# Optimization experiments

Measured on AMD Instinct MI355X. Metric: run time of the kernel, lower is better.

The kernel has to match this reference:

```python
import jax, jax.numpy as jnp
import numpy as np
from jax import lax

B, NBB, C, H, W = 32, 16, 1024, 22, 22
P = 3            # pooled output size (3x3)
SCALE = 1.0 / 16.0
EPS = 1e-5


def setup_inputs() -> dict:
    key = jax.random.key(0)
    ks = jax.random.split(key, 12)
    feat = jax.random.normal(ks[0], (B, C, H, W), jnp.float32)
    # bbox in xywh image coords, in-range for a 352x352 search region
    xy = jax.random.uniform(ks[1], (B, NBB, 2), jnp.float32, 0.0, 250.0)
    wh = jax.random.uniform(ks[2], (B, NBB, 2), jnp.float32, 16.0, 100.0)
    bbox = jnp.concatenate([xy, wh], axis=-1)
    conv_w = jax.random.normal(ks[3], (C, C, 3, 3), jnp.float32) * 0.01
    conv_b = jnp.zeros((C,), jnp.float32)
    bn_gamma = jnp.ones((C,), jnp.float32)
    bn_beta = jnp.zeros((C,), jnp.float32)
    bn_mean = jax.random.normal(ks[4], (C,), jnp.float32) * 0.1
    bn_var = jax.random.uniform(ks[5], (C,), jnp.float32, 0.5, 1.5)
    w1 = jax.random.normal(ks[6], (C // 2, C), jnp.float32) * 0.02
    b1 = jnp.zeros((C // 2,), jnp.float32)
    w2 = jax.random.normal(ks[7], (C // 2, C // 2), jnp.float32) * 0.02
    b2 = jnp.zeros((C // 2,), jnp.float32)
    w3 = jax.random.normal(ks[8], (512, C // 2), jnp.float32) * 0.02
    b3 = jnp.zeros((512,), jnp.float32)
    return dict(feat=feat, bbox=bbox, conv_w=conv_w, conv_b=conv_b,
                bn_gamma=bn_gamma, bn_beta=bn_beta, bn_mean=bn_mean, bn_var=bn_var,
                w1=w1, b1=b1, w2=w2, b2=b2, w3=w3, b3=b3)


def _hat_int(t):
    # Antiderivative of the bilinear hat h(u)=max(0,1-|u|), clipped to support.
    t = jnp.clip(t, -1.0, 1.0)
    return t + 0.5 - 0.5 * t * jnp.abs(t)


def _bin_weights(lo, bw, n):
    # lo, bw: [B, NBB].  Returns exact integral weights [B, NBB, P, n]:
    # W[b,r,p,i] = integral over bin p of hat(x - i) dx  (PrRoI closed form).
    p = jnp.arange(P, dtype=lo.dtype)
    xs = lo[..., None] + p * bw[..., None]          # [B,NBB,P] bin starts
    xe = xs + bw[..., None]                          # bin ends
    i = jnp.arange(n, dtype=lo.dtype)
    return _hat_int(xe[..., None] - i) - _hat_int(xs[..., None] - i)


def reference(feat, bbox, conv_w, conv_b, bn_gamma, bn_beta, bn_mean, bn_var,
              w1, b1, w2, b2, w3, b3):
    # --- PrRoI pooling (exact separable bilinear integral) ---
    x1 = bbox[..., 0] * SCALE
    y1 = bbox[..., 1] * SCALE
    x2 = (bbox[..., 0] + bbox[..., 2]) * SCALE
    y2 = (bbox[..., 1] + bbox[..., 3]) * SCALE
    bw = (x2 - x1) / P
    bh = (y2 - y1) / P
    Wx = _bin_weights(x1, bw, W)                     # [B,NBB,P,W]
    Wy = _bin_weights(y1, bh, H)                     # [B,NBB,P,H]
    pooled = jnp.einsum('bchw,bnqh,bnpw->bncqp', feat, Wy, Wx)  # [B,NBB,C,P,P]
    area = jnp.maximum(bw * bh, 0.0)[..., None, None, None]
    pooled = jnp.where(area > 0, pooled / jnp.maximum(area, 1e-12), 0.0)
    x = pooled.reshape(B * NBB, C, P, P)

    # --- conv_bn_relu: 3x3 conv, valid padding -> 1x1, BN (eval), ReLU ---
    x = lax.conv_general_dilated(x, conv_w, (1, 1), 'VALID',
                                 dimension_numbers=('NCHW', 'OIHW', 'NCHW'))
    x = x + conv_b[:, None, None]
    x = (x - bn_mean[:, None, None]) * (bn_gamma * lax.rsqrt(bn_var + EPS))[:, None, None]
    x = x + bn_beta[:, None, None]
    x = jax.nn.relu(x)

    # --- MLP head ---
    x = x.reshape(B * NBB, C)
    x = jax.nn.relu(x @ w1.T + b1)
    x = jax.nn.relu(x @ w2.T + b2)
    x = x @ w3.T + b3
    return x.reshape(B, NBB, 512)
```

## Files before the change

### kernel.cpp

```cpp
#include <hip/hip_runtime.h>
#include <hip/hip_bf16.h>

#define B_    32
#define NBB_  16
#define C_    1024
#define NROI  512
#define KCONV 9216
#define SCALE_ (1.0f/16.0f)
#define EPS_  1e-5f

using f32x4  = __attribute__((ext_vector_type(4))) float;
using bf16x8 = __attribute__((ext_vector_type(8))) short;

__device__ __forceinline__ unsigned f2bf(float f) {
  union { float f; unsigned u; } x; x.f = f;
  unsigned r = x.u + 0x7fffu + ((x.u >> 16) & 1u);
  return r >> 16;
}

__device__ __forceinline__ unsigned pk_bf16(float lo, float hi) {
  __hip_bfloat162 h = __float22bfloat162_rn(make_float2(lo, hi));
  return *reinterpret_cast<unsigned*>(&h);
}

__device__ __forceinline__ float hat_int(float t) {
  t = fminf(fmaxf(t, -1.f), 1.f);
  return t + 0.5f - 0.5f * t * fabsf(t);
}

__device__ __forceinline__ void glds16(const void* g, void* l) {
  __builtin_amdgcn_global_load_lds((const __attribute__((address_space(1))) void*)g,
                                   (__attribute__((address_space(3))) void*)l, 16, 0, 0);
}

__global__ __launch_bounds__(192) void prep_w2d(const float* __restrict__ bbox,
                                                unsigned short* __restrict__ W2d) {
  __shared__ float wyS[16*66], wxS[16*66];
  int b = blockIdx.x, tid = threadIdx.x;
  for (int t = tid; t < 352; t += 192) {
    int n = t / 22, i = t - n * 22;
    float4 bb = ((const float4*)bbox)[b*16 + n];
    float x1 = bb.x * SCALE_, y1 = bb.y * SCALE_;
    float x2 = (bb.x + bb.z) * SCALE_, y2 = (bb.y + bb.w) * SCALE_;
    float bw = (x2 - x1) / 3.f, bh = (y2 - y1) / 3.f;
    float area = fmaxf(bw * bh, 0.f);
    float inv = area > 0.f ? 1.f / fmaxf(area, 1e-12f) : 0.f;
    float fi = (float)i;
#pragma unroll
    for (int q = 0; q < 3; ++q) {
      float sy = y1 + q * bh;
      wyS[n*66 + q*22 + i] = hat_int(sy + bh - fi) - hat_int(sy - fi);
      float sx = x1 + q * bw;
      wxS[n*66 + q*22 + i] = (hat_int(sx + bw - fi) - hat_int(sx - fi)) * inv;
    }
  }
  __syncthreads();
  if (tid < 144) {
    int n = tid / 9, qp = tid - n*9, q = qp / 3, p = qp - q*3;
    const float* wyp = wyS + n*66 + q*22;
    const float* wxp = wxS + n*66 + p*22;
    unsigned short* out = W2d + ((size_t)b*144 + tid) * 512;
    for (int h = 0; h < 22; ++h) {
      float yv = wyp[h];
      int kb = h * 22;
#pragma unroll
      for (int w = 0; w < 22; w += 2)
        *(unsigned*)&out[kb + w] = pk_bf16(yv * wxp[w], yv * wxp[w+1]);
    }
#pragma unroll
    for (int k = 484; k < 512; k += 2) *(unsigned*)&out[k] = 0u;
  }
}

__global__ __launch_bounds__(256) void cvt3_bf16(const float* __restrict__ w1, const float* __restrict__ w2,
                                                 const float* __restrict__ w3,
                                                 unsigned short* __restrict__ o1, unsigned short* __restrict__ o2,
                                                 unsigned short* __restrict__ o3) {
  int i = blockIdx.x * 256 + threadIdx.x;
  const float* src; unsigned short* dst; int g;
  if (i < 65536)      { src = w1; dst = o1; g = i; }
  else if (i < 98304) { src = w2; dst = o2; g = i - 65536; }
  else                { src = w3; dst = o3; g = i - 98304; }
  float4 a = ((const float4*)src)[2*g];
  float4 b = ((const float4*)src)[2*g + 1];
  uint4 pk;
  pk.x = pk_bf16(a.x, a.y); pk.y = pk_bf16(a.z, a.w);
  pk.z = pk_bf16(b.x, b.y); pk.w = pk_bf16(b.z, b.w);
  ((uint4*)dst)[g] = pk;
}

__global__ __launch_bounds__(256) void convw_t(const float* __restrict__ cw,
                                               unsigned short* __restrict__ out) {
  __shared__ unsigned short T[9][1028];
  int o = blockIdx.x, tid = threadIdx.x;
  const float4* src = (const float4*)(cw + (size_t)o * 9216);
#pragma unroll
  for (int it = 0; it < 9; ++it) {
    int i = tid + it * 256;
    float4 v = src[i];
    int e = i * 4;
    { int c = e / 9,     qp = e - c*9;             T[qp][c] = (unsigned short)f2bf(v.x); }
    { int ee = e+1; int c = ee / 9, qp = ee - c*9; T[qp][c] = (unsigned short)f2bf(v.y); }
    { int ee = e+2; int c = ee / 9, qp = ee - c*9; T[qp][c] = (unsigned short)f2bf(v.z); }
    { int ee = e+3; int c = ee / 9, qp = ee - c*9; T[qp][c] = (unsigned short)f2bf(v.w); }
  }
  __syncthreads();
  unsigned short* dst = out + (size_t)o * 9216;
#pragma unroll
  for (int qp = 0; qp < 9; ++qp) {
    uint2 w = *(const uint2*)&T[qp][tid * 4];
    ((uint2*)(dst + qp * 1024))[tid] = w;
  }
}

__global__ __launch_bounds__(256) void cvt_feat(const float* __restrict__ feat,
                                                unsigned short* __restrict__ featB) {
  int blk = blockIdx.x;
  int tid = threadIdx.x;
  const float4* src = (const float4*)(feat + (size_t)blk * 16 * 484);
  unsigned short* dstB = featB + (size_t)blk * 16 * 512;
#pragma unroll
  for (int it = 0; it < 8; ++it) {
    int j = tid + it * 256;
    if (j < 1936) {
      float4 v = src[j];
      int lin = j * 4;
      int c = lin / 484, w = lin - c * 484;
      uint2 pk;
      pk.x = pk_bf16(v.x, v.y); pk.y = pk_bf16(v.z, v.w);
      *(uint2*)&dstB[(size_t)c * 512 + w] = pk;
    }
  }
  if (tid < 112) {
    int c = tid / 7, ws = tid - c * 7;
    uint2 z; z.x = 0u; z.y = 0u;
    *(uint2*)&dstB[(size_t)c * 512 + 484 + ws * 4] = z;
  }
}

__global__ __launch_bounds__(384) void pool_gemm(const unsigned short* __restrict__ W2d,
                                                 const unsigned short* __restrict__ featB,
                                                 unsigned short* __restrict__ X) {
  __shared__ __align__(16) unsigned short As[2][4608];
  __shared__ __align__(16) unsigned short Bs[2][4096];
  int tid = threadIdx.x;
  int nt = blockIdx.x, b = blockIdx.y;
  int lane = tid & 63, wid = tid >> 6;
  int wm = wid >> 1, wn = wid & 1;
  int l15 = lane & 15, kg = lane >> 4;
  const unsigned short* aBase = W2d  + (size_t)b * 144 * 512;
  const unsigned short* bBase = featB + ((size_t)b * 1024 + (size_t)nt * 128) * 512;
  f32x4 acc[3][4] = {};

#define ISSUEP(buf, s) do { int k0_ = (s) * 32; \
    _Pragma("unroll") for (int ii = 0; ii < 3; ++ii) { \
      int sb = ii*384 + wid*64; \
      if (sb < 1088) { \
        int slot = sb + lane; \
        if (sb < 576) { \
          int row = slot >> 2, seg = (slot & 3) ^ ((row >> 1) & 3); \
          glds16(aBase + (size_t)row*512 + k0_ + seg*8, (char*)&As[(buf)][0] + sb*16); \
        } else { \
          int s2 = slot - 576; int row = s2 >> 2, seg = (s2 & 3) ^ ((row >> 1) & 3); \
          glds16(bBase + (size_t)row*512 + k0_ + seg*8, (char*)&Bs[(buf)][0] + (sb-576)*16); \
        } } } } while (0)

  ISSUEP(0, 0);
  int cur = 0;
  for (int s = 0; s < 16; ++s) {
    __syncthreads();
    if (s < 15) ISSUEP(cur ^ 1, s + 1);
    bf16x8 af[3], bfr[4];
#pragma unroll
    for (int fm = 0; fm < 3; ++fm) {
      int r = wm*48 + fm*16 + l15;
      af[fm] = *(const bf16x8*)&As[cur][r*32 + ((kg ^ ((r >> 1) & 3)) << 3)];
    }
#pragma unroll
    for (int fn = 0; fn < 4; ++fn) {
      int r = wn*64 + fn*16 + l15;
      bfr[fn] = *(const bf16x8*)&Bs[cur][r*32 + ((kg ^ ((r >> 1) & 3)) << 3)];
    }
#pragma unroll
    for (int fm = 0; fm < 3; ++fm)
#pragma unroll
      for (int fn = 0; fn < 4; ++fn)
        acc[fm][fn] = __builtin_amdgcn_mfma_f32_16x16x32_bf16(af[fm], bfr[fn], acc[fm][fn], 0, 0, 0);
    cur ^= 1;
  }
#undef ISSUEP

#pragma unroll
  for (int fm = 0; fm < 3; ++fm)
#pragma unroll
    for (int r = 0; r < 4; ++r) {
      int m = wm*48 + fm*16 + kg*4 + r;
      int n = m / 9, qp = m - n*9;
      size_t base = ((size_t)(b*16 + n)) * KCONV + (size_t)qp * 1024 + (size_t)nt * 128;
#pragma unroll
      for (int fn = 0; fn < 4; ++fn)
        X[base + wn*64 + fn*16 + l15] = (unsigned short)f2bf(acc[fm][fn][r]);
    }
}

__global__ __launch_bounds__(256) void gemm128(const unsigned short* __restrict__ A,
                                               const unsigned short* __restrict__ Bm,
                                               float* __restrict__ Cp,
                                               int M, int N, int K, int kChunk) {
  __shared__ __align__(16) unsigned short As[2][4096];
  __shared__ __align__(16) unsigned short Bs[2][4096];
  int tid = threadIdx.x;
  int lane = tid & 63, wid = tid >> 6;
  int wm = wid >> 1, wn = wid & 1;
  int l15 = lane & 15, kg = lane >> 4;
  int nt = blockIdx.x, mt = blockIdx.y, z = blockIdx.z;
  int kbeg = z * kChunk;
  int steps = kChunk / 32;

  int row0 = tid >> 2, row1 = 64 + row0;
  int slot = tid & 3;
  int s0 = slot ^ ((row0 >> 1) & 3);
  int s1 = slot ^ ((row1 >> 1) & 3);
  const unsigned short* ga0 = A  + (size_t)(mt*128 + row0) * K + kbeg + s0*8;
  const unsigned short* ga1 = A  + (size_t)(mt*128 + row1) * K + kbeg + s1*8;
  const unsigned short* gb0 = Bm + (size_t)(nt*128 + row0) * K + kbeg + s0*8;
  const unsigned short* gb1 = Bm + (size_t)(nt*128 + row1) * K + kbeg + s1*8;
  int wbyte = wid * 1024;

  f32x4 acc[4][4] = {};
  int cur = 0;

#define ISSUE(buf, s) do { int ko = (s) * 32; \
    glds16(ga0 + ko, (char*)&As[(buf)][0] + wbyte); \
    glds16(ga1 + ko, (char*)&As[(buf)][0] + 4096 + wbyte); \
    glds16(gb0 + ko, (char*)&Bs[(buf)][0] + wbyte); \
    glds16(gb1 + ko, (char*)&Bs[(buf)][0] + 4096 + wbyte); } while (0)

  ISSUE(0, 0);
  for (int s = 0; s < steps; ++s) {
    __syncthreads();
    if (s + 1 < steps) ISSUE(cur ^ 1, s + 1);
    bf16x8 af[4], bfr[4];
#pragma unroll
    for (int fm = 0; fm < 4; ++fm) {
      int fr = wm*64 + fm*16 + l15;
      af[fm] = *(const bf16x8*)&As[cur][fr*32 + ((kg ^ ((fr >> 1) & 3)) << 3)];
    }
#pragma unroll
    for (int fn = 0; fn < 4; ++fn) {
      int fr = wn*64 + fn*16 + l15;
      bfr[fn] = *(const bf16x8*)&Bs[cur][fr*32 + ((kg ^ ((fr >> 1) & 3)) << 3)];
    }
#pragma unroll
    for (int fm = 0; fm < 4; ++fm)
#pragma unroll
      for (int fn = 0; fn < 4; ++fn)
        acc[fm][fn] = __builtin_amdgcn_mfma_f32_16x16x32_bf16(af[fm], bfr[fn], acc[fm][fn], 0, 0, 0);
    cur ^= 1;
  }
#undef ISSUE

  float* cp = Cp + ((size_t)z * M + (size_t)mt * 128) * N + (size_t)nt * 128;
#pragma unroll
  for (int fm = 0; fm < 4; ++fm)
#pragma unroll
    for (int fn = 0; fn < 4; ++fn)
#pragma unroll
      for (int r = 0; r < 4; ++r) {
        int row = wm*64 + fm*16 + kg*4 + r;
        int col = wn*64 + fn*16 + l15;
        cp[(size_t)row * N + col] = acc[fm][fn][r];
      }
}

__global__ __launch_bounds__(256) void gemm_nt(const unsigned short* __restrict__ A,
                                               const unsigned short* __restrict__ Bm,
                                               float* __restrict__ Cp,
                                               int M, int N, int K, int kChunk) {
  __shared__ __align__(16) unsigned short As[64][40];
  __shared__ __align__(16) unsigned short Bs[64][40];
  int tid = threadIdx.x;
  int lane = tid & 63, wid = tid >> 6;
  int wm = wid >> 1, wn = wid & 1;
  int l15 = lane & 15, kg = lane >> 4;
  int nt = blockIdx.x, mt = blockIdx.y, z = blockIdx.z;
  int kbeg = z * kChunk;
  int kend = kbeg + kChunk; if (kend > K) kend = K;
  int srow = tid >> 2, sseg = tid & 3;
  const unsigned short* aG = A  + (size_t)(mt*64 + srow) * K + sseg * 8;
  const unsigned short* bG = Bm + (size_t)(nt*64 + srow) * K + sseg * 8;
  f32x4 acc[2][2] = {};

  for (int k0 = kbeg; k0 < kend; k0 += 32) {
    uint4 av = *(const uint4*)(aG + k0);
    uint4 bv = *(const uint4*)(bG + k0);
    __syncthreads();
    *(uint4*)&As[srow][sseg*8] = av;
    *(uint4*)&Bs[srow][sseg*8] = bv;
    __syncthreads();
    bf16x8 a0 = *(const bf16x8*)&As[wm*32 +      l15][kg*8];
    bf16x8 a1 = *(const bf16x8*)&As[wm*32 + 16 + l15][kg*8];
    bf16x8 b0 = *(const bf16x8*)&Bs[wn*32 +      l15][kg*8];
    bf16x8 b1 = *(const bf16x8*)&Bs[wn*32 + 16 + l15][kg*8];
    acc[0][0] = __builtin_amdgcn_mfma_f32_16x16x32_bf16(a0, b0, acc[0][0], 0, 0, 0);
    acc[0][1] = __builtin_amdgcn_mfma_f32_16x16x32_bf16(a0, b1, acc[0][1], 0, 0, 0);
    acc[1][0] = __builtin_amdgcn_mfma_f32_16x16x32_bf16(a1, b0, acc[1][0], 0, 0, 0);
    acc[1][1] = __builtin_amdgcn_mfma_f32_16x16x32_bf16(a1, b1, acc[1][1], 0, 0, 0);
  }

  float* cp = Cp + ((size_t)z * M + (size_t)mt * 64) * N + (size_t)nt * 64;
#pragma unroll
  for (int fm = 0; fm < 2; ++fm)
#pragma unroll
    for (int fn = 0; fn < 2; ++fn)
#pragma unroll
      for (int r = 0; r < 4; ++r) {
        int row = wm*32 + fm*16 + kg*4 + r;
        int col = wn*32 + fn*16 + l15;
        cp[(size_t)row * N + col] = acc[fm][fn][r];
      }
}

template<int MODE>
__global__ __launch_bounds__(256) void epi(const float* __restrict__ Cp, int SK, int MN4, int N,
                                           const float* __restrict__ bias,
                                           const float* __restrict__ g,
                                           const float* __restrict__ be,
                                           const float* __restrict__ mu,
                                           const float* __restrict__ var,
                                           unsigned short* __restrict__ outb,
                                           float* __restrict__ outf) {
  int i = blockIdx.x * 256 + threadIdx.x;
  if (i >= MN4) return;
  float4 s = ((const float4*)Cp)[i];
  for (int z = 1; z < SK; ++z) {
    float4 t = ((const float4*)Cp)[(size_t)z * MN4 + i];
    s.x += t.x; s.y += t.y; s.z += t.z; s.w += t.w;
  }
  int n0 = (i * 4) % N;
  float v[4] = {s.x, s.y, s.z, s.w};
  if (MODE == 0) {
    float o[4];
#pragma unroll
    for (int j = 0; j < 4; ++j) {
      int n = n0 + j;
      float sc = g[n] * rsqrtf(var[n] + EPS_);
      o[j] = fmaxf((v[j] + bias[n] - mu[n]) * sc + be[n], 0.f);
    }
    uint2 pk; pk.x = pk_bf16(o[0], o[1]); pk.y = pk_bf16(o[2], o[3]);
    *(uint2*)&outb[(size_t)i * 4] = pk;
  } else if (MODE == 1) {
    uint2 pk;
    pk.x = pk_bf16(fmaxf(v[0] + bias[n0], 0.f),   fmaxf(v[1] + bias[n0+1], 0.f));
    pk.y = pk_bf16(fmaxf(v[2] + bias[n0+2], 0.f), fmaxf(v[3] + bias[n0+3], 0.f));
    *(uint2*)&outb[(size_t)i * 4] = pk;
  } else {
    float4 o;
    o.x = v[0] + bias[n0];     o.y = v[1] + bias[n0 + 1];
    o.z = v[2] + bias[n0 + 2]; o.w = v[3] + bias[n0 + 3];
    ((float4*)outf)[i] = o;
  }
}

extern "C" void kernel_launch(void* const* d_in, const int* in_sizes, int n_in,
                              void* d_out, int out_size, void* d_ws, size_t ws_size,
                              hipStream_t stream) {
  const float* feat   = (const float*)d_in[0];
  const float* bbox   = (const float*)d_in[1];
  const float* conv_w = (const float*)d_in[2];
  const float* conv_b = (const float*)d_in[3];
  const float* gamma  = (const float*)d_in[4];
  const float* beta   = (const float*)d_in[5];
  const float* mean   = (const float*)d_in[6];
  const float* var    = (const float*)d_in[7];
  const float* w1     = (const float*)d_in[8];
  const float* b1     = (const float*)d_in[9];
  const float* w2     = (const float*)d_in[10];
  const float* b2     = (const float*)d_in[11];
  const float* w3     = (const float*)d_in[12];
  const float* b3     = (const float*)d_in[13];

  char* ws = (char*)d_ws;
  unsigned short* W2d  = (unsigned short*)(ws);
  unsigned short* featB= (unsigned short*)(ws + 4718592);
  float*          part = (float*)(ws);
  unsigned short* H0   = (unsigned short*)(ws + 16777216);
  unsigned short* H1   = (unsigned short*)(ws + 17825792);
  unsigned short* H2   = (unsigned short*)(ws + 18350080);
  unsigned short* Xb   = (unsigned short*)(ws + 38273024);
  unsigned short* Wfb  = (unsigned short*)(ws + 47710208);
  unsigned short* w1b  = (unsigned short*)(ws + 66584576);
  unsigned short* w2b  = (unsigned short*)(ws + 67633152);
  unsigned short* w3b  = (unsigned short*)(ws + 68157440);

  prep_w2d<<<32, 192, 0, stream>>>(bbox, W2d);
  convw_t<<<1024, 256, 0, stream>>>(conv_w, Wfb);
  cvt3_bf16<<<512, 256, 0, stream>>>(w1, w2, w3, w1b, w2b, w3b);
  cvt_feat<<<2048, 256, 0, stream>>>(feat, featB);

  pool_gemm<<<dim3(8, 32), 384, 0, stream>>>(W2d, featB, Xb);

  gemm128<<<dim3(8, 4, 8), 256, 0, stream>>>(Xb, Wfb, part, 512, 1024, 9216, 1152);
  epi<0><<<(131072 + 255) / 256, 256, 0, stream>>>(part, 8, 131072, 1024,
      conv_b, gamma, beta, mean, var, H0, nullptr);

  gemm_nt<<<dim3(8, 8, 4), 256, 0, stream>>>(H0, w1b, part, 512, 512, 1024, 256);
  epi<1><<<(65536 + 255) / 256, 256, 0, stream>>>(part, 4, 65536, 512,
      b1, nullptr, nullptr, nullptr, nullptr, H1, nullptr);

  gemm_nt<<<dim3(8, 8, 4), 256, 0, stream>>>(H1, w2b, part, 512, 512, 512, 128);
  epi<1><<<(65536 + 255) / 256, 256, 0, stream>>>(part, 4, 65536, 512,
      b2, nullptr, nullptr, nullptr, nullptr, H2, nullptr);

  gemm_nt<<<dim3(8, 8, 4), 256, 0, stream>>>(H2, w3b, part, 512, 512, 512, 128);
  epi<2><<<(65536 + 255) / 256, 256, 0, stream>>>(part, 4, 65536, 512,
      b3, nullptr, nullptr, nullptr, nullptr, nullptr, (float*)d_out);
}
```

Baseline: 130.5 us.

## Merge prep kernels and fuse conv GEMM and MLP into one cooperative kernel

Combines the four preprocessing kernels into a single launch that dispatches on block index. Replaces the conv GEMM, its split-K reduction epilogue, and the three MLP GEMM and epilogue pairs with one persistent cooperative kernel of 256 blocks, separated by grid-wide syncs. This is meant to remove many kernel launches and the gaps between them. The cost is several grid.sync barriers, and the cooperative launch needs all 256 blocks to be resident at once.

```diff
diff --git a/kernel.cpp b/kernel.cpp
--- a/kernel.cpp
+++ b/kernel.cpp
@@ -1,5 +1,8 @@
 #include <hip/hip_runtime.h>
 #include <hip/hip_bf16.h>
+#include <hip/hip_cooperative_groups.h>
+
+namespace cg = cooperative_groups;
 
 #define B_    32
 #define NBB_  16
@@ -33,108 +36,110 @@
                                    (__attribute__((address_space(3))) void*)l, 16, 0, 0);
 }
 
-__global__ __launch_bounds__(192) void prep_w2d(const float* __restrict__ bbox,
-                                                unsigned short* __restrict__ W2d) {
-  __shared__ float wyS[16*66], wxS[16*66];
-  int b = blockIdx.x, tid = threadIdx.x;
-  for (int t = tid; t < 352; t += 192) {
-    int n = t / 22, i = t - n * 22;
-    float4 bb = ((const float4*)bbox)[b*16 + n];
-    float x1 = bb.x * SCALE_, y1 = bb.y * SCALE_;
-    float x2 = (bb.x + bb.z) * SCALE_, y2 = (bb.y + bb.w) * SCALE_;
-    float bw = (x2 - x1) / 3.f, bh = (y2 - y1) / 3.f;
-    float area = fmaxf(bw * bh, 0.f);
-    float inv = area > 0.f ? 1.f / fmaxf(area, 1e-12f) : 0.f;
-    float fi = (float)i;
-#pragma unroll
-    for (int q = 0; q < 3; ++q) {
-      float sy = y1 + q * bh;
-      wyS[n*66 + q*22 + i] = hat_int(sy + bh - fi) - hat_int(sy - fi);
-      float sx = x1 + q * bw;
-      wxS[n*66 + q*22 + i] = (hat_int(sx + bw - fi) - hat_int(sx - fi)) * inv;
-    }
-  }
-  __syncthreads();
-  if (tid < 144) {
-    int n = tid / 9, qp = tid - n*9, q = qp / 3, p = qp - q*3;
-    const float* wyp = wyS + n*66 + q*22;
-    const float* wxp = wxS + n*66 + p*22;
-    unsigned short* out = W2d + ((size_t)b*144 + tid) * 512;
-    for (int h = 0; h < 22; ++h) {
-      float yv = wyp[h];
-      int kb = h * 22;
-#pragma unroll
-      for (int w = 0; w < 22; w += 2)
-        *(unsigned*)&out[kb + w] = pk_bf16(yv * wxp[w], yv * wxp[w+1]);
-    }
-#pragma unroll
-    for (int k = 484; k < 512; k += 2) *(unsigned*)&out[k] = 0u;
-  }
-}
-
-__global__ __launch_bounds__(256) void cvt3_bf16(const float* __restrict__ w1, const float* __restrict__ w2,
-                                                 const float* __restrict__ w3,
-                                                 unsigned short* __restrict__ o1, unsigned short* __restrict__ o2,
-                                                 unsigned short* __restrict__ o3) {
-  int i = blockIdx.x * 256 + threadIdx.x;
-  const float* src; unsigned short* dst; int g;
-  if (i < 65536)      { src = w1; dst = o1; g = i; }
-  else if (i < 98304) { src = w2; dst = o2; g = i - 65536; }
-  else                { src = w3; dst = o3; g = i - 98304; }
-  float4 a = ((const float4*)src)[2*g];
-  float4 b = ((const float4*)src)[2*g + 1];
-  uint4 pk;
-  pk.x = pk_bf16(a.x, a.y); pk.y = pk_bf16(a.z, a.w);
-  pk.z = pk_bf16(b.x, b.y); pk.w = pk_bf16(b.z, b.w);
-  ((uint4*)dst)[g] = pk;
-}
-
-__global__ __launch_bounds__(256) void convw_t(const float* __restrict__ cw,
-                                               unsigned short* __restrict__ out) {
-  __shared__ unsigned short T[9][1028];
-  int o = blockIdx.x, tid = threadIdx.x;
-  const float4* src = (const float4*)(cw + (size_t)o * 9216);
-#pragma unroll
-  for (int it = 0; it < 9; ++it) {
-    int i = tid + it * 256;
-    float4 v = src[i];
-    int e = i * 4;
-    { int c = e / 9,     qp = e - c*9;             T[qp][c] = (unsigned short)f2bf(v.x); }
-    { int ee = e+1; int c = ee / 9, qp = ee - c*9; T[qp][c] = (unsigned short)f2bf(v.y); }
-    { int ee = e+2; int c = ee / 9, qp = ee - c*9; T[qp][c] = (unsigned short)f2bf(v.z); }
-    { int ee = e+3; int c = ee / 9, qp = ee - c*9; T[qp][c] = (unsigned short)f2bf(v.w); }
-  }
-  __syncthreads();
-  unsigned short* dst = out + (size_t)o * 9216;
-#pragma unroll
-  for (int qp = 0; qp < 9; ++qp) {
-    uint2 w = *(const uint2*)&T[qp][tid * 4];
-    ((uint2*)(dst + qp * 1024))[tid] = w;
-  }
-}
-
-__global__ __launch_bounds__(256) void cvt_feat(const float* __restrict__ feat,
-                                                unsigned short* __restrict__ featB) {
-  int blk = blockIdx.x;
+__global__ __launch_bounds__(256) void prep_all(
+    const float* __restrict__ bbox, const float* __restrict__ feat,
+    const float* __restrict__ conv_w,
+    const float* __restrict__ w1, const float* __restrict__ w2, const float* __restrict__ w3,
+    unsigned short* __restrict__ W2d, unsigned short* __restrict__ featB,
+    unsigned short* __restrict__ Wfb,
+    unsigned short* __restrict__ o1, unsigned short* __restrict__ o2,
+    unsigned short* __restrict__ o3)
+{
+  __shared__ __align__(16) char psm[18504];
   int tid = threadIdx.x;
-  const float4* src = (const float4*)(feat + (size_t)blk * 16 * 484);
-  unsigned short* dstB = featB + (size_t)blk * 16 * 512;
-#pragma unroll
-  for (int it = 0; it < 8; ++it) {
-    int j = tid + it * 256;
-    if (j < 1936) {
-      float4 v = src[j];
-      int lin = j * 4;
-      int c = lin / 484, w = lin - c * 484;
-      uint2 pk;
-      pk.x = pk_bf16(v.x, v.y); pk.y = pk_bf16(v.z, v.w);
-      *(uint2*)&dstB[(size_t)c * 512 + w] = pk;
-    }
-  }
-  if (tid < 112) {
-    int c = tid / 7, ws = tid - c * 7;
-    uint2 z; z.x = 0u; z.y = 0u;
-    *(uint2*)&dstB[(size_t)c * 512 + 484 + ws * 4] = z;
+  int bx = blockIdx.x;
+
+  if (bx < 32) {
+    int b = bx;
+    float* wyS = (float*)psm;
+    float* wxS = wyS + 1056;
+    for (int t = tid; t < 352; t += 256) {
+      int n = t / 22, i = t - n * 22;
+      float4 bb = ((const float4*)bbox)[b*16 + n];
+      float x1 = bb.x * SCALE_, y1 = bb.y * SCALE_;
+      float x2 = (bb.x + bb.z) * SCALE_, y2 = (bb.y + bb.w) * SCALE_;
+      float bw = (x2 - x1) / 3.f, bh = (y2 - y1) / 3.f;
+      float area = fmaxf(bw * bh, 0.f);
+      float inv = area > 0.f ? 1.f / fmaxf(area, 1e-12f) : 0.f;
+      float fi = (float)i;
+#pragma unroll
+      for (int q = 0; q < 3; ++q) {
+        float sy = y1 + q * bh;
+        wyS[n*66 + q*22 + i] = hat_int(sy + bh - fi) - hat_int(sy - fi);
+        float sx = x1 + q * bw;
+        wxS[n*66 + q*22 + i] = (hat_int(sx + bw - fi) - hat_int(sx - fi)) * inv;
+      }
+    }
+    __syncthreads();
+    if (tid < 144) {
+      int n = tid / 9, qp = tid - n*9, q = qp / 3, p = qp - q*3;
+      const float* wyp = wyS + n*66 + q*22;
+      const float* wxp = wxS + n*66 + p*22;
+      unsigned short* out = W2d + ((size_t)b*144 + tid) * 512;
+      for (int h = 0; h < 22; ++h) {
+        float yv = wyp[h];
+        int kb = h * 22;
+#pragma unroll
+        for (int w = 0; w < 22; w += 2)
+          *(unsigned*)&out[kb + w] = pk_bf16(yv * wxp[w], yv * wxp[w+1]);
+      }
+#pragma unroll
+      for (int k = 484; k < 512; k += 2) *(unsigned*)&out[k] = 0u;
+    }
+  } else if (bx < 2080) {
+    int blk = bx - 32;
+    const float4* src = (const float4*)(feat + (size_t)blk * 16 * 484);
+    unsigned short* dstB = featB + (size_t)blk * 16 * 512;
+#pragma unroll
+    for (int it = 0; it < 8; ++it) {
+      int j = tid + it * 256;
+      if (j < 1936) {
+        float4 v = src[j];
+        int lin = j * 4;
+        int c = lin / 484, w = lin - c * 484;
+        uint2 pk;
+        pk.x = pk_bf16(v.x, v.y); pk.y = pk_bf16(v.z, v.w);
+        *(uint2*)&dstB[(size_t)c * 512 + w] = pk;
+      }
+    }
+    if (tid < 112) {
+      int c = tid / 7, wsl = tid - c * 7;
+      uint2 z; z.x = 0u; z.y = 0u;
+      *(uint2*)&dstB[(size_t)c * 512 + 484 + wsl * 4] = z;
+    }
+  } else if (bx < 3104) {
+    int o = bx - 2080;
+    unsigned short (*T)[1028] = (unsigned short(*)[1028])psm;
+    const float4* src = (const float4*)(conv_w + (size_t)o * 9216);
+#pragma unroll
+    for (int it = 0; it < 9; ++it) {
+      int i = tid + it * 256;
+      float4 v = src[i];
+      int e = i * 4;
+      { int c = e / 9,     qp = e - c*9;             T[qp][c] = (unsigned short)f2bf(v.x); }
+      { int ee = e+1; int c = ee / 9, qp = ee - c*9; T[qp][c] = (unsigned short)f2bf(v.y); }
+      { int ee = e+2; int c = ee / 9, qp = ee - c*9; T[qp][c] = (unsigned short)f2bf(v.z); }
+      { int ee = e+3; int c = ee / 9, qp = ee - c*9; T[qp][c] = (unsigned short)f2bf(v.w); }
+    }
+    __syncthreads();
+    unsigned short* dst = Wfb + (size_t)o * 9216;
+#pragma unroll
+    for (int qp = 0; qp < 9; ++qp) {
+      uint2 w = *(const uint2*)&T[qp][tid * 4];
+      ((uint2*)(dst + qp * 1024))[tid] = w;
+    }
+  } else {
+    int i = (bx - 3104) * 256 + tid;
+    const float* src; unsigned short* dst; int g;
+    if (i < 65536)      { src = w1; dst = o1; g = i; }
+    else if (i < 98304) { src = w2; dst = o2; g = i - 65536; }
+    else                { src = w3; dst = o3; g = i - 98304; }
+    float4 a = ((const float4*)src)[2*g];
+    float4 b = ((const float4*)src)[2*g + 1];
+    uint4 pk;
+    pk.x = pk_bf16(a.x, a.y); pk.y = pk_bf16(a.z, a.w);
+    pk.z = pk_bf16(b.x, b.y); pk.w = pk_bf16(b.z, b.w);
+    ((uint4*)dst)[g] = pk;
   }
 }
 
@@ -203,89 +208,17 @@
     }
 }
 
-__global__ __launch_bounds__(256) void gemm128(const unsigned short* __restrict__ A,
-                                               const unsigned short* __restrict__ Bm,
-                                               float* __restrict__ Cp,
-                                               int M, int N, int K, int kChunk) {
-  __shared__ __align__(16) unsigned short As[2][4096];
-  __shared__ __align__(16) unsigned short Bs[2][4096];
-  int tid = threadIdx.x;
+__device__ __forceinline__ void mlp_gemm(const unsigned short* __restrict__ A,
+                                         const unsigned short* __restrict__ Bm,
+                                         float* __restrict__ Cp,
+                                         int K, int kChunk, int blk, int tid, char* smem) {
+  unsigned short* AsB = (unsigned short*)smem;
+  unsigned short* BsB = (unsigned short*)(smem + 5120);
   int lane = tid & 63, wid = tid >> 6;
   int wm = wid >> 1, wn = wid & 1;
   int l15 = lane & 15, kg = lane >> 4;
-  int nt = blockIdx.x, mt = blockIdx.y, z = blockIdx.z;
-  int kbeg = z * kChunk;
-  int steps = kChunk / 32;
-
-  int row0 = tid >> 2, row1 = 64 + row0;
-  int slot = tid & 3;
-  int s0 = slot ^ ((row0 >> 1) & 3);
-  int s1 = slot ^ ((row1 >> 1) & 3);
-  const unsigned short* ga0 = A  + (size_t)(mt*128 + row0) * K + kbeg + s0*8;
-  const unsigned short* ga1 = A  + (size_t)(mt*128 + row1) * K + kbeg + s1*8;
-  const unsigned short* gb0 = Bm + (size_t)(nt*128 + row0) * K + kbeg + s0*8;
-  const unsigned short* gb1 = Bm + (size_t)(nt*128 + row1) * K + kbeg + s1*8;
-  int wbyte = wid * 1024;
-
-  f32x4 acc[4][4] = {};
-  int cur = 0;
-
-#define ISSUE(buf, s) do { int ko = (s) * 32; \
-    glds16(ga0 + ko, (char*)&As[(buf)][0] + wbyte); \
-    glds16(ga1 + ko, (char*)&As[(buf)][0] + 4096 + wbyte); \
-    glds16(gb0 + ko, (char*)&Bs[(buf)][0] + wbyte); \
-    glds16(gb1 + ko, (char*)&Bs[(buf)][0] + 4096 + wbyte); } while (0)
-
-  ISSUE(0, 0);
-  for (int s = 0; s < steps; ++s) {
-    __syncthreads();
-    if (s + 1 < steps) ISSUE(cur ^ 1, s + 1);
-    bf16x8 af[4], bfr[4];
-#pragma unroll
-    for (int fm = 0; fm < 4; ++fm) {
-      int fr = wm*64 + fm*16 + l15;
-      af[fm] = *(const bf16x8*)&As[cur][fr*32 + ((kg ^ ((fr >> 1) & 3)) << 3)];
-    }
-#pragma unroll
-    for (int fn = 0; fn < 4; ++fn) {
-      int fr = wn*64 + fn*16 + l15;
-      bfr[fn] = *(const bf16x8*)&Bs[cur][fr*32 + ((kg ^ ((fr >> 1) & 3)) << 3)];
-    }
-#pragma unroll
-    for (int fm = 0; fm < 4; ++fm)
-#pragma unroll
-      for (int fn = 0; fn < 4; ++fn)
-        acc[fm][fn] = __builtin_amdgcn_mfma_f32_16x16x32_bf16(af[fm], bfr[fn], acc[fm][fn], 0, 0, 0);
-    cur ^= 1;
-  }
-#undef ISSUE
-
-  float* cp = Cp + ((size_t)z * M + (size_t)mt * 128) * N + (size_t)nt * 128;
-#pragma unroll
-  for (int fm = 0; fm < 4; ++fm)
-#pragma unroll
-    for (int fn = 0; fn < 4; ++fn)
-#pragma unroll
-      for (int r = 0; r < 4; ++r) {
-        int row = wm*64 + fm*16 + kg*4 + r;
-        int col = wn*64 + fn*16 + l15;
-        cp[(size_t)row * N + col] = acc[fm][fn][r];
-      }
-}
-
-__global__ __launch_bounds__(256) void gemm_nt(const unsigned short* __restrict__ A,
-                                               const unsigned short* __restrict__ Bm,
-                                               float* __restrict__ Cp,
-                                               int M, int N, int K, int kChunk) {
-  __shared__ __align__(16) unsigned short As[64][40];
-  __shared__ __align__(16) unsigned short Bs[64][40];
-  int tid = threadIdx.x;
-  int lane = tid & 63, wid = tid >> 6;
-  int wm = wid >> 1, wn = wid & 1;
-  int l15 = lane & 15, kg = lane >> 4;
-  int nt = blockIdx.x, mt = blockIdx.y, z = blockIdx.z;
-  int kbeg = z * kChunk;
-  int kend = kbeg + kChunk; if (kend > K) kend = K;
+  int nt = blk & 7, mt = (blk >> 3) & 7, z = blk >> 6;
+  int kbeg = z * kChunk, kend = kbeg + kChunk;
   int srow = tid >> 2, sseg = tid & 3;
   const unsigned short* aG = A  + (size_t)(mt*64 + srow) * K + sseg * 8;
   const unsigned short* bG = Bm + (size_t)(nt*64 + srow) * K + sseg * 8;
@@ -295,20 +228,20 @@
     uint4 av = *(const uint4*)(aG + k0);
     uint4 bv = *(const uint4*)(bG + k0);
     __syncthreads();
-    *(uint4*)&As[srow][sseg*8] = av;
-    *(uint4*)&Bs[srow][sseg*8] = bv;
+    *(uint4*)&AsB[srow*40 + sseg*8] = av;
+    *(uint4*)&BsB[srow*40 + sseg*8] = bv;
     __syncthreads();
-    bf16x8 a0 = *(const bf16x8*)&As[wm*32 +      l15][kg*8];
-    bf16x8 a1 = *(const bf16x8*)&As[wm*32 + 16 + l15][kg*8];
-    bf16x8 b0 = *(const bf16x8*)&Bs[wn*32 +      l15][kg*8];
-    bf16x8 b1 = *(const bf16x8*)&Bs[wn*32 + 16 + l15][kg*8];
+    bf16x8 a0 = *(const bf16x8*)&AsB[(wm*32 +      l15)*40 + kg*8];
+    bf16x8 a1 = *(const bf16x8*)&AsB[(wm*32 + 16 + l15)*40 + kg*8];
+    bf16x8 b0 = *(const bf16x8*)&BsB[(wn*32 +      l15)*40 + kg*8];
+    bf16x8 b1 = *(const bf16x8*)&BsB[(wn*32 + 16 + l15)*40 + kg*8];
     acc[0][0] = __builtin_amdgcn_mfma_f32_16x16x32_bf16(a0, b0, acc[0][0], 0, 0, 0);
     acc[0][1] = __builtin_amdgcn_mfma_f32_16x16x32_bf16(a0, b1, acc[0][1], 0, 0, 0);
     acc[1][0] = __builtin_amdgcn_mfma_f32_16x16x32_bf16(a1, b0, acc[1][0], 0, 0, 0);
     acc[1][1] = __builtin_amdgcn_mfma_f32_16x16x32_bf16(a1, b1, acc[1][1], 0, 0, 0);
   }
 
-  float* cp = Cp + ((size_t)z * M + (size_t)mt * 64) * N + (size_t)nt * 64;
+  float* cp = Cp + ((size_t)z * 512 + (size_t)mt * 64) * 512 + (size_t)nt * 64;
 #pragma unroll
   for (int fm = 0; fm < 2; ++fm)
 #pragma unroll
@@ -317,49 +250,153 @@
       for (int r = 0; r < 4; ++r) {
         int row = wm*32 + fm*16 + kg*4 + r;
         int col = wn*32 + fn*16 + l15;
-        cp[(size_t)row * N + col] = acc[fm][fn][r];
-      }
-}
-
-template<int MODE>
-__global__ __launch_bounds__(256) void epi(const float* __restrict__ Cp, int SK, int MN4, int N,
-                                           const float* __restrict__ bias,
-                                           const float* __restrict__ g,
-                                           const float* __restrict__ be,
-                                           const float* __restrict__ mu,
-                                           const float* __restrict__ var,
-                                           unsigned short* __restrict__ outb,
-                                           float* __restrict__ outf) {
-  int i = blockIdx.x * 256 + threadIdx.x;
-  if (i >= MN4) return;
+        cp[(size_t)row * 512 + col] = acc[fm][fn][r];
+      }
+}
+
+__device__ __forceinline__ void red4(const float* __restrict__ Cp, int i,
+                                     const float* __restrict__ bias,
+                                     unsigned short* __restrict__ outb,
+                                     float* __restrict__ outf) {
   float4 s = ((const float4*)Cp)[i];
-  for (int z = 1; z < SK; ++z) {
-    float4 t = ((const float4*)Cp)[(size_t)z * MN4 + i];
+#pragma unroll
+  for (int z2 = 1; z2 < 4; ++z2) {
+    float4 t = ((const float4*)Cp)[(size_t)z2 * 65536 + i];
     s.x += t.x; s.y += t.y; s.z += t.z; s.w += t.w;
   }
-  int n0 = (i * 4) % N;
-  float v[4] = {s.x, s.y, s.z, s.w};
-  if (MODE == 0) {
-    float o[4];
-#pragma unroll
-    for (int j = 0; j < 4; ++j) {
-      int n = n0 + j;
-      float sc = g[n] * rsqrtf(var[n] + EPS_);
-      o[j] = fmaxf((v[j] + bias[n] - mu[n]) * sc + be[n], 0.f);
-    }
-    uint2 pk; pk.x = pk_bf16(o[0], o[1]); pk.y = pk_bf16(o[2], o[3]);
-    *(uint2*)&outb[(size_t)i * 4] = pk;
-  } else if (MODE == 1) {
+  int n0 = (i * 4) & 511;
+  if (outb) {
     uint2 pk;
-    pk.x = pk_bf16(fmaxf(v[0] + bias[n0], 0.f),   fmaxf(v[1] + bias[n0+1], 0.f));
-    pk.y = pk_bf16(fmaxf(v[2] + bias[n0+2], 0.f), fmaxf(v[3] + bias[n0+3], 0.f));
+    pk.x = pk_bf16(fmaxf(s.x + bias[n0], 0.f),   fmaxf(s.y + bias[n0+1], 0.f));
+    pk.y = pk_bf16(fmaxf(s.z + bias[n0+2], 0.f), fmaxf(s.w + bias[n0+3], 0.f));
     *(uint2*)&outb[(size_t)i * 4] = pk;
   } else {
     float4 o;
-    o.x = v[0] + bias[n0];     o.y = v[1] + bias[n0 + 1];
-    o.z = v[2] + bias[n0 + 2]; o.w = v[3] + bias[n0 + 3];
+    o.x = s.x + bias[n0];   o.y = s.y + bias[n0+1];
+    o.z = s.z + bias[n0+2]; o.w = s.w + bias[n0+3];
     ((float4*)outf)[i] = o;
   }
+}
+
+__global__ __launch_bounds__(256) void conv_tail(
+    const unsigned short* __restrict__ Xb, const unsigned short* __restrict__ Wfb,
+    const unsigned short* __restrict__ w1b, const unsigned short* __restrict__ w2b,
+    const unsigned short* __restrict__ w3b,
+    float* __restrict__ part,
+    unsigned short* __restrict__ H0, unsigned short* __restrict__ H1,
+    unsigned short* __restrict__ H2,
+    const float* __restrict__ conv_b, const float* __restrict__ gamma,
+    const float* __restrict__ beta, const float* __restrict__ mu,
+    const float* __restrict__ var,
+    const float* __restrict__ b1, const float* __restrict__ b2,
+    const float* __restrict__ b3, float* __restrict__ outF)
+{
+  __shared__ __align__(16) char smem[32768];
+  cg::grid_group grid = cg::this_grid();
+  int tid = threadIdx.x, blk = blockIdx.x;
+  int lane = tid & 63, wid = tid >> 6;
+  int wm = wid >> 1, wn = wid & 1;
+  int l15 = lane & 15, kg = lane >> 4;
+
+  {
+    const int K = KCONV, N = 1024, M = 512;
+    int nt = blk & 7, mt = (blk >> 3) & 3, z = blk >> 5;
+    int kbeg = z * 1152;
+    int row0 = tid >> 2, row1 = 64 + row0;
+    int slot = tid & 3;
+    int s0 = slot ^ ((row0 >> 1) & 3);
+    int s1 = slot ^ ((row1 >> 1) & 3);
+    const unsigned short* ga0 = Xb  + (size_t)(mt*128 + row0) * K + kbeg + s0*8;
+    const unsigned short* ga1 = Xb  + (size_t)(mt*128 + row1) * K + kbeg + s1*8;
+    const unsigned short* gb0 = Wfb + (size_t)(nt*128 + row0) * K + kbeg + s0*8;
+    const unsigned short* gb1 = Wfb + (size_t)(nt*128 + row1) * K + kbeg + s1*8;
+    int wbyte = wid * 1024;
+    unsigned short* AsB = (unsigned short*)smem;
+    unsigned short* BsB = (unsigned short*)(smem + 16384);
+    f32x4 acc[4][4] = {};
+    int cur = 0;
+
+#define ISSUE(buf, s) do { int ko = (s) * 32; \
+    glds16(ga0 + ko, (char*)AsB + (buf)*8192 + wbyte); \
+    glds16(ga1 + ko, (char*)AsB + (buf)*8192 + 4096 + wbyte); \
+    glds16(gb0 + ko, (char*)BsB + (buf)*8192 + wbyte); \
+    glds16(gb1 + ko, (char*)BsB + (buf)*8192 + 4096 + wbyte); } while (0)
+
+    ISSUE(0, 0);
+    for (int s = 0; s < 36; ++s) {
+      __syncthreads();
+      if (s + 1 < 36) ISSUE(cur ^ 1, s + 1);
+      bf16x8 af[4], bfr[4];
+#pragma unroll
+      for (int fm = 0; fm < 4; ++fm) {
+        int fr = wm*64 + fm*16 + l15;
+        af[fm] = *(const bf16x8*)&AsB[cur*4096 + fr*32 + ((kg ^ ((fr >> 1) & 3)) << 3)];
+      }
+#pragma unroll
+      for (int fn = 0; fn < 4; ++fn) {
+        int fr = wn*64 + fn*16 + l15;
+        bfr[fn] = *(const bf16x8*)&BsB[cur*4096 + fr*32 + ((kg ^ ((fr >> 1) & 3)) << 3)];
+      }
+#pragma unroll
+      for (int fm = 0; fm < 4; ++fm)
+#pragma unroll
+        for (int fn = 0; fn < 4; ++fn)
+          acc[fm][fn] = __builtin_amdgcn_mfma_f32_16x16x32_bf16(af[fm], bfr[fn], acc[fm][fn], 0, 0, 0);
+      cur ^= 1;
+    }
+#undef ISSUE
+
+    float* cp = part + ((size_t)z * M + (size_t)mt * 128) * N + (size_t)nt * 128;
+#pragma unroll
+    for (int fm = 0; fm < 4; ++fm)
+#pragma unroll
+      for (int fn = 0; fn < 4; ++fn)
+#pragma unroll
+        for (int r = 0; r < 4; ++r) {
+          int row = wm*64 + fm*16 + kg*4 + r;
+          int col = wn*64 + fn*16 + l15;
+          cp[(size_t)row * N + col] = acc[fm][fn][r];
+        }
+  }
+  __threadfence(); grid.sync();
+
+  {
+#pragma unroll
+    for (int rep = 0; rep < 2; ++rep) {
+      int i = blk * 256 + tid + rep * 65536;
+      float4 s = ((const float4*)part)[i];
+#pragma unroll
+      for (int z2 = 1; z2 < 8; ++z2) {
+        float4 t = ((const float4*)part)[(size_t)z2 * 131072 + i];
+        s.x += t.x; s.y += t.y; s.z += t.z; s.w += t.w;
+      }
+      int n0 = (i * 4) & 1023;
+      float o[4] = {s.x, s.y, s.z, s.w};
+#pragma unroll
+      for (int j = 0; j < 4; ++j) {
+        int n = n0 + j;
+        float sc = gamma[n] * rsqrtf(var[n] + EPS_);
+        o[j] = fmaxf((o[j] + conv_b[n] - mu[n]) * sc + beta[n], 0.f);
+      }
+      uint2 pk; pk.x = pk_bf16(o[0], o[1]); pk.y = pk_bf16(o[2], o[3]);
+      *(uint2*)&H0[(size_t)i * 4] = pk;
+    }
+  }
+  __threadfence(); grid.sync();
+
+  mlp_gemm(H0, w1b, part, 1024, 256, blk, tid, smem);
+  __threadfence(); grid.sync();
+  red4(part, blk * 256 + tid, b1, H1, nullptr);
+  __threadfence(); grid.sync();
+
+  mlp_gemm(H1, w2b, part, 512, 128, blk, tid, smem);
+  __threadfence(); grid.sync();
+  red4(part, blk * 256 + tid, b2, H2, nullptr);
+  __threadfence(); grid.sync();
+
+  mlp_gemm(H2, w3b, part, 512, 128, blk, tid, smem);
+  __threadfence(); grid.sync();
+  red4(part, blk * 256 + tid, b3, nullptr, outF);
 }
 
 extern "C" void kernel_launch(void* const* d_in, const int* in_sizes, int n_in,
@@ -393,26 +430,15 @@
   unsigned short* w2b  = (unsigned short*)(ws + 67633152);
   unsigned short* w3b  = (unsigned short*)(ws + 68157440);
 
-  prep_w2d<<<32, 192, 0, stream>>>(bbox, W2d);
-  convw_t<<<1024, 256, 0, stream>>>(conv_w, Wfb);
-  cvt3_bf16<<<512, 256, 0, stream>>>(w1, w2, w3, w1b, w2b, w3b);
-  cvt_feat<<<2048, 256, 0, stream>>>(feat, featB);
+  prep_all<<<3616, 256, 0, stream>>>(bbox, feat, conv_w, w1, w2, w3,
+                                     W2d, featB, Wfb, w1b, w2b, w3b);
 
   pool_gemm<<<dim3(8, 32), 384, 0, stream>>>(W2d, featB, Xb);
 
-  gemm128<<<dim3(8, 4, 8), 256, 0, stream>>>(Xb, Wfb, part, 512, 1024, 9216, 1152);
-  epi<0><<<(131072 + 255) / 256, 256, 0, stream>>>(part, 8, 131072, 1024,
-      conv_b, gamma, beta, mean, var, H0, nullptr);
-
-  gemm_nt<<<dim3(8, 8, 4), 256, 0, stream>>>(H0, w1b, part, 512, 512, 1024, 256);
-  epi<1><<<(65536 + 255) / 256, 256, 0, stream>>>(part, 4, 65536, 512,
-      b1, nullptr, nullptr, nullptr, nullptr, H1, nullptr);
-
-  gemm_nt<<<dim3(8, 8, 4), 256, 0, stream>>>(H1, w2b, part, 512, 512, 512, 128);
-  epi<1><<<(65536 + 255) / 256, 256, 0, stream>>>(part, 4, 65536, 512,
-      b2, nullptr, nullptr, nullptr, nullptr, H2, nullptr);
-
-  gemm_nt<<<dim3(8, 8, 4), 256, 0, stream>>>(H2, w3b, part, 512, 512, 512, 128);
-  epi<2><<<(65536 + 255) / 256, 256, 0, stream>>>(part, 4, 65536, 512,
-      b3, nullptr, nullptr, nullptr, nullptr, nullptr, (float*)d_out);
-}
+  float* outF = (float*)d_out;
+  void* args[] = {(void*)&Xb, (void*)&Wfb, (void*)&w1b, (void*)&w2b, (void*)&w3b,
+                  (void*)&part, (void*)&H0, (void*)&H1, (void*)&H2,
+                  (void*)&conv_b, (void*)&gamma, (void*)&beta, (void*)&mean, (void*)&var,
+                  (void*)&b1, (void*)&b2, (void*)&b3, (void*)&outF};
+  hipLaunchCooperativeKernel((const void*)conv_tail, dim3(256), dim3(256), args, 0, stream);
+}
```

After: 493.0 us. +277.9%, slower.
